# Kernel tuning notes

Hardware: AMD Instinct MI355X
Metric: run time of the kernel (lower is better)

The kernel has to match this reference:

```python
import jax, jax.numpy as jnp
import numpy as np

D, H, WIN, TEMP = 512, 8, 2, 1.0
DH = D // H
SCALE = DH ** -0.5
SHIFT = WIN // 2


def _ln(x, g, b):
    m = jnp.mean(x, -1, keepdims=True)
    v = jnp.mean(jnp.square(x - m), -1, keepdims=True)
    return (x - m) * jax.lax.rsqrt(v + 1e-5) * g + b


def _win_attn(q, k, v):
    a = jax.nn.softmax(jnp.einsum('nhqd,nhkd->nhqk', q * SCALE, k) / TEMP, axis=-1)
    return jnp.einsum('nhqk,nhkd->nhqd', a, v)


def _self_block(x, p):
    qkv_w, qkv_b, proj_w, proj_b, n1g, n1b, n2g, n2b = p
    b, t, d = x.shape
    sc = x
    xw = _ln(x, n1g, n1b).reshape(b * t // WIN, WIN, d)  # window partition
    qkv = (xw @ qkv_w + qkv_b).reshape(-1, WIN, 3, H, DH).transpose(2, 0, 3, 1, 4)
    o = _win_attn(qkv[0], qkv[1], qkv[2])
    o = o.transpose(0, 2, 1, 3).reshape(-1, WIN, d) @ proj_w + proj_b
    return _ln(o.reshape(b, t, d) + sc, n2g, n2b)  # window reverse + residual


def _self_tf(x, p):
    x = _self_block(x, p)
    x = jnp.roll(x, -SHIFT, axis=1)   # sequence_shift
    x = _self_block(x, p)
    return jnp.roll(x, SHIFT, axis=1)  # sequence_inverse_shift


def _cross_block(x, y, p):
    q_w, q_b, kv_w, kv_b, proj_w, proj_b, n1g, n1b, n2g, n2b = p
    b, t, d = x.shape
    sc = x
    xw = _ln(x, n1g, n1b).reshape(-1, WIN, d)
    yw = _ln(y, n1g, n1b).reshape(-1, WIN, d)  # shared pre_norm, as in source
    q = (xw @ q_w + q_b).reshape(-1, WIN, H, DH).transpose(0, 2, 1, 3)
    kv = (yw @ kv_w + kv_b).reshape(-1, WIN, 2, H, DH).transpose(2, 0, 3, 1, 4)
    o = _win_attn(q, kv[0], kv[1])
    o = o.transpose(0, 2, 1, 3).reshape(-1, WIN, d) @ proj_w + proj_b
    return _ln(o.reshape(b, t, d) + sc, n2g, n2b)


def _cross_tf(x, y, p):
    x = _cross_block(x, y, p)
    x = jnp.roll(x, -SHIFT, axis=1)
    x = _cross_block(x, jnp.roll(y, -SHIFT, axis=1), p)
    return jnp.roll(x, SHIFT, axis=1)


def setup_inputs() -> dict:
    key = jax.random.key(0)
    ks = iter(jax.random.split(key, 40))
    B, T = 16, 4096
    d = {
        'x': jax.random.normal(next(ks), (B, T, D), jnp.float32),
        'y': jax.random.normal(next(ks), (B, T, D), jnp.float32),
    }

    def w(shape):
        return jax.random.normal(next(ks), shape, jnp.float32) * 0.02

    for m in ('wa', 'wv'):  # within-modal audio / video
        d[m + '_qkv_w'] = w((D, 3 * D)); d[m + '_qkv_b'] = jnp.zeros((3 * D,), jnp.float32)
        d[m + '_proj_w'] = w((D, D));    d[m + '_proj_b'] = jnp.zeros((D,), jnp.float32)
        d[m + '_n1_g'] = jnp.ones((D,), jnp.float32); d[m + '_n1_b'] = jnp.zeros((D,), jnp.float32)
        d[m + '_n2_g'] = jnp.ones((D,), jnp.float32); d[m + '_n2_b'] = jnp.zeros((D,), jnp.float32)
    # shared cross-modal transformer
    d['cm_q_w'] = w((D, D));      d['cm_q_b'] = jnp.zeros((D,), jnp.float32)
    d['cm_kv_w'] = w((D, 2 * D)); d['cm_kv_b'] = jnp.zeros((2 * D,), jnp.float32)
    d['cm_proj_w'] = w((D, D));   d['cm_proj_b'] = jnp.zeros((D,), jnp.float32)
    d['cm_n1_g'] = jnp.ones((D,), jnp.float32); d['cm_n1_b'] = jnp.zeros((D,), jnp.float32)
    d['cm_n2_g'] = jnp.ones((D,), jnp.float32); d['cm_n2_b'] = jnp.zeros((D,), jnp.float32)
    return d


def reference(x, y,
              wa_qkv_w, wa_qkv_b, wa_proj_w, wa_proj_b, wa_n1_g, wa_n1_b, wa_n2_g, wa_n2_b,
              wv_qkv_w, wv_qkv_b, wv_proj_w, wv_proj_b, wv_n1_g, wv_n1_b, wv_n2_g, wv_n2_b,
              cm_q_w, cm_q_b, cm_kv_w, cm_kv_b, cm_proj_w, cm_proj_b, cm_n1_g, cm_n1_b, cm_n2_g, cm_n2_b):
    pa = (wa_qkv_w, wa_qkv_b, wa_proj_w, wa_proj_b, wa_n1_g, wa_n1_b, wa_n2_g, wa_n2_b)
    pv = (wv_qkv_w, wv_qkv_b, wv_proj_w, wv_proj_b, wv_n1_g, wv_n1_b, wv_n2_g, wv_n2_b)
    pc = (cm_q_w, cm_q_b, cm_kv_w, cm_kv_b, cm_proj_w, cm_proj_b, cm_n1_g, cm_n1_b, cm_n2_g, cm_n2_b)
    # args.s1_attn == 'all' path
    x = _self_tf(x, pa)
    y = _self_tf(y, pv)
    xc = _cross_tf(x, y, pc)
    yc = _cross_tf(y, x, pc)
    return jnp.stack([x + xc, y + yc])  # (2, B, T, D)
```

## Files before the change

### kernel.cpp

```cpp
#include <hip/hip_runtime.h>

typedef unsigned short u16;
typedef unsigned int u32;
typedef __attribute__((ext_vector_type(8))) short short8;
typedef __attribute__((ext_vector_type(4))) short short4v;
typedef __attribute__((ext_vector_type(4))) float f32x4;

#define D_MODEL 512
#define NH 8
#define TSEQ 4096
#define NB 16
#define NROWS (NB*TSEQ)
#define QK_SCALE 0.125f
#define KDIM 512
#define NKI (KDIM/32)

__device__ __forceinline__ float b2f(u16 u){
    union { float f; unsigned int i; } v; v.i = ((unsigned int)u) << 16; return v.f;
}
__device__ __forceinline__ u16 f2b(float f){
    union { float f; unsigned int i; } v; v.f = f;
    unsigned int r = v.i + 0x7FFFu + ((v.i >> 16) & 1u);
    return (u16)(r >> 16);
}

__device__ __forceinline__ void async_copy16(u16* lds, const u16* g){
    __builtin_amdgcn_global_load_lds(
        (const __attribute__((address_space(1))) u32*)g,
        (__attribute__((address_space(3))) u32*)lds, 16, 0, 0);
}

__global__ void wconv_kernel(const float* __restrict__ W, u16* __restrict__ Wt, int K, int N){
    int idx = blockIdx.x * 256 + threadIdx.x;
    if (idx >= K * N) return;
    int n = idx / K;
    int k = idx - n * K;
    Wt[idx] = f2b(W[(size_t)k * N + n]);
}

__global__ __launch_bounds__(256) void ln_kernel(
    const float* __restrict__ X, const float* __restrict__ g,
    const float* __restrict__ b, u16* __restrict__ out)
{
    int row  = blockIdx.x * 4 + (threadIdx.x >> 6);
    int lane = threadIdx.x & 63;
    size_t base = (size_t)row * D_MODEL + lane * 8;
    float4 x0 = *(const float4*)(X + base);
    float4 x1 = *(const float4*)(X + base + 4);
    float t[8] = {x0.x,x0.y,x0.z,x0.w,x1.x,x1.y,x1.z,x1.w};
    float s = 0.f, ss = 0.f;
    #pragma unroll
    for (int j = 0; j < 8; j++){ s += t[j]; ss += t[j]*t[j]; }
    #pragma unroll
    for (int m = 1; m < 64; m <<= 1){ s += __shfl_xor(s, m); ss += __shfl_xor(ss, m); }
    float mean = s * (1.f/D_MODEL);
    float var  = ss * (1.f/D_MODEL) - mean*mean;
    float rst  = rsqrtf(var + 1e-5f);
    float4 g0 = *(const float4*)(g + lane*8);
    float4 g1 = *(const float4*)(g + lane*8 + 4);
    float4 c0 = *(const float4*)(b + lane*8);
    float4 c1 = *(const float4*)(b + lane*8 + 4);
    float gv[8] = {g0.x,g0.y,g0.z,g0.w,g1.x,g1.y,g1.z,g1.w};
    float bv[8] = {c0.x,c0.y,c0.z,c0.w,c1.x,c1.y,c1.z,c1.w};
    short8 o;
    #pragma unroll
    for (int j = 0; j < 8; j++) o[j] = (short)f2b((t[j]-mean)*rst*gv[j] + bv[j]);
    *(short8*)(out + base) = o;
}

__global__ __launch_bounds__(256) void resln_kernel(
    const u16* __restrict__ P, const float* __restrict__ Xin,
    const float* __restrict__ Add,
    const float* __restrict__ g, const float* __restrict__ b,
    float* __restrict__ out,
    u16* __restrict__ lnout, const float* __restrict__ g2, const float* __restrict__ b2)
{
    int row  = blockIdx.x * 4 + (threadIdx.x >> 6);
    int lane = threadIdx.x & 63;
    size_t base = (size_t)row * D_MODEL + lane * 8;
    short8 pv = *(const short8*)(P + base);
    float4 x0 = *(const float4*)(Xin + base);
    float4 x1 = *(const float4*)(Xin + base + 4);
    float xr[8] = {x0.x,x0.y,x0.z,x0.w,x1.x,x1.y,x1.z,x1.w};
    float t[8];
    #pragma unroll
    for (int j = 0; j < 8; j++) t[j] = b2f((u16)pv[j]) + xr[j];
    float s = 0.f, ss = 0.f;
    #pragma unroll
    for (int j = 0; j < 8; j++){ s += t[j]; ss += t[j]*t[j]; }
    #pragma unroll
    for (int m = 1; m < 64; m <<= 1){ s += __shfl_xor(s, m); ss += __shfl_xor(ss, m); }
    float mean = s * (1.f/D_MODEL);
    float var  = ss * (1.f/D_MODEL) - mean*mean;
    float rst  = rsqrtf(var + 1e-5f);
    float4 g0 = *(const float4*)(g + lane*8);
    float4 g1 = *(const float4*)(g + lane*8 + 4);
    float4 c0 = *(const float4*)(b + lane*8);
    float4 c1 = *(const float4*)(b + lane*8 + 4);
    float gv[8] = {g0.x,g0.y,g0.z,g0.w,g1.x,g1.y,g1.z,g1.w};
    float bv[8] = {c0.x,c0.y,c0.z,c0.w,c1.x,c1.y,c1.z,c1.w};
    float o[8];
    #pragma unroll
    for (int j = 0; j < 8; j++) o[j] = (t[j]-mean)*rst*gv[j] + bv[j];

    if (lnout){
        float s2 = 0.f, ss2 = 0.f;
        #pragma unroll
        for (int j = 0; j < 8; j++){ s2 += o[j]; ss2 += o[j]*o[j]; }
        #pragma unroll
        for (int m = 1; m < 64; m <<= 1){ s2 += __shfl_xor(s2, m); ss2 += __shfl_xor(ss2, m); }
        float mean2 = s2 * (1.f/D_MODEL);
        float var2  = ss2 * (1.f/D_MODEL) - mean2*mean2;
        float rst2  = rsqrtf(var2 + 1e-5f);
        float4 g20 = *(const float4*)(g2 + lane*8);
        float4 g21 = *(const float4*)(g2 + lane*8 + 4);
        float4 b20 = *(const float4*)(b2 + lane*8);
        float4 b21 = *(const float4*)(b2 + lane*8 + 4);
        float g2v[8] = {g20.x,g20.y,g20.z,g20.w,g21.x,g21.y,g21.z,g21.w};
        float b2v[8] = {b20.x,b20.y,b20.z,b20.w,b21.x,b21.y,b21.z,b21.w};
        short8 lo;
        #pragma unroll
        for (int j = 0; j < 8; j++) lo[j] = (short)f2b((o[j]-mean2)*rst2*g2v[j] + b2v[j]);
        *(short8*)(lnout + base) = lo;
    }
    if (Add){
        float4 a0 = *(const float4*)(Add + base);
        float4 a1 = *(const float4*)(Add + base + 4);
        float av[8] = {a0.x,a0.y,a0.z,a0.w,a1.x,a1.y,a1.z,a1.w};
        #pragma unroll
        for (int j = 0; j < 8; j++) o[j] += av[j];
    }
    float4 r0 = {o[0],o[1],o[2],o[3]};
    float4 r1 = {o[4],o[5],o[6],o[7]};
    *(float4*)(out + base)     = r0;
    *(float4*)(out + base + 4) = r1;
}

__global__ __launch_bounds__(256) void qkvattn_kernel(
    const u16* __restrict__ A, const u16* __restrict__ Wt,
    const float* __restrict__ bias, u16* __restrict__ O, int shift)
{
    __shared__ __align__(16) u16 lds[2][20*512];
    int tid  = threadIdx.x;
    int lane = tid & 63;
    int wid  = tid >> 6;

    int bid  = blockIdx.x;
    int swz  = (bid & 7) * 512 + (bid >> 3);
    int head = swz >> 9;
    int rt   = swz & 511;
    int bt   = rt >> 5;
    int tb   = (rt & 31) * 128;

    f32x4 acc[2][12];
    f32x4 zero = {0.f,0.f,0.f,0.f};
    #pragma unroll
    for (int m = 0; m < 2; m++)
        #pragma unroll
        for (int n = 0; n < 12; n++) acc[m][n] = zero;

    int rr = lane >> 2, kc = (lane & 3) * 8;
    const u16* p[5];
    int cidb = wid * 5;
    #pragma unroll
    for (int q = 0; q < 5; q++){
        int cid = cidb + q;
        if (cid < 8){
            int i   = cid*16 + rr;
            int tok = (tb + shift + i) & (TSEQ-1);
            p[q] = A + ((size_t)bt * TSEQ + tok) * KDIM + kc;
        } else {
            int cb   = cid - 8;
            int wrow = (cb >> 2) * 512 + head*64 + (cb & 3)*16 + rr;
            p[q] = Wt + (size_t)wrow * KDIM + kc;
        }
    }

    int lrow = lane & 15;
    int lk   = (lane >> 4) * 8;
    int aoff = (wid*32 + lrow) * 32 + lk;
    int boff = 8*512 + lrow*32 + lk;

    #pragma unroll
    for (int q = 0; q < 5; q++){ async_copy16(&lds[0][(cidb+q)*512], p[q]); p[q] += 32; }
    asm volatile("s_waitcnt vmcnt(0)" ::: "memory");
    __syncthreads();

    #pragma unroll
    for (int t = 0; t < NKI; t++){
        const u16* cbuf = lds[t & 1];
        u16* nbuf = (u16*)lds[(t & 1) ^ 1];
        if (t < NKI-1){
            #pragma unroll
            for (int q = 0; q < 5; q++){ async_copy16(&nbuf[(cidb+q)*512], p[q]); p[q] += 32; }
        }
        short8 af[2], bf[12];
        #pragma unroll
        for (int m = 0; m < 2; m++) af[m] = *(const short8*)(cbuf + aoff + m*512);
        #pragma unroll
        for (int n = 0; n < 12; n++) bf[n] = *(const short8*)(cbuf + boff + n*512);
        #pragma unroll
        for (int m = 0; m < 2; m++)
            #pragma unroll
            for (int n = 0; n < 12; n++)
                acc[m][n] = __builtin_amdgcn_mfma_f32_16x16x32_bf16(af[m], bf[n], acc[m][n], 0, 0, 0);
        if (t < NKI-1){
            asm volatile("s_waitcnt vmcnt(0)" ::: "memory");
            __syncthreads();
        }
    }

    int g_ = lane >> 4, lc = lane & 15;
    float bq[4], bk[4], bv[4];
    #pragma unroll
    for (int n = 0; n < 4; n++){
        int d = head*64 + n*16 + lc;
        bq[n] = bias[d]; bk[n] = bias[512 + d]; bv[n] = bias[1024 + d];
    }
    #pragma unroll
    for (int m = 0; m < 2; m++){
        #pragma unroll
        for (int wnd = 0; wnd < 2; wnd++){
            int ja = 2*wnd, jb = ja + 1;
            float s00=0.f, s01=0.f, s10=0.f, s11=0.f;
            #pragma unroll
            for (int n = 0; n < 4; n++){
                float qa = acc[m][n][ja] + bq[n],  qb = acc[m][n][jb] + bq[n];
                float ka = acc[m][4+n][ja] + bk[n], kb = acc[m][4+n][jb] + bk[n];
                s00 += qa*ka; s01 += qa*kb; s10 += qb*ka; s11 += qb*kb;
            }
            #pragma unroll
            for (int msk = 1; msk < 16; msk <<= 1){
                s00 += __shfl_xor(s00, msk); s01 += __shfl_xor(s01, msk);
                s10 += __shfl_xor(s10, msk); s11 += __shfl_xor(s11, msk);
            }
            s00 *= QK_SCALE; s01 *= QK_SCALE; s10 *= QK_SCALE; s11 *= QK_SCALE;
            float m0 = fmaxf(s00, s01), m1 = fmaxf(s10, s11);
            float e00 = expf(s00-m0), e01 = expf(s01-m0);
            float e10 = expf(s10-m1), e11 = expf(s11-m1);
            float ia = 1.f/(e00+e01), ib = 1.f/(e10+e11);
            float a00 = e00*ia, a01 = e01*ia, a10 = e10*ib, a11 = e11*ib;
            int ra = wid*32 + m*16 + 4*g_ + ja;
            int ta = (tb + shift + ra) & (TSEQ-1);
            size_t growa = (size_t)bt * TSEQ + ta;
            size_t growb = (size_t)bt * TSEQ + ((ta + 1) & (TSEQ-1));
            #pragma unroll
            for (int n = 0; n < 4; n++){
                float va = acc[m][8+n][ja] + bv[n], vb = acc[m][8+n][jb] + bv[n];
                int col = head*64 + n*16 + lc;
                O[growa * D_MODEL + col] = f2b(a00*va + a01*vb);
                O[growb * D_MODEL + col] = f2b(a10*va + a11*vb);
            }
        }
    }
}

#define AOFc(buf,h) (((buf)*2+(h))*8192)
#define BOFc(buf,h) (32768 + ((buf)*2+(h))*8192)

__global__ __launch_bounds__(512, 2) void gemm256_kernel(
    const u16* __restrict__ A, const u16* __restrict__ Wt,
    const float* __restrict__ bias, u16* __restrict__ C, int N, int nN)
{
    __shared__ __align__(16) u16 sh[65536];
    u16* sh_ = (u16*)sh;
    const int tid = threadIdx.x, lane = tid & 63, wid = tid >> 6;
    const int wm = wid >> 2, wn = wid & 3;
    const int cpx = (int)gridDim.x >> 3;
    const int swz = ((int)blockIdx.x & 7) * cpx + ((int)blockIdx.x >> 3);
    const int row0 = (swz / nN) * 256;
    const int col0 = (swz % nN) * 256;

    f32x4 acc[8][4];
    f32x4 zero = {0.f,0.f,0.f,0.f};
    #pragma unroll
    for (int m = 0; m < 8; m++)
        #pragma unroll
        for (int n = 0; n < 4; n++) acc[m][n] = zero;

    const int lrow = lane & 15, khi = lane >> 4;
    const int swx   = (lrow & 4) << 2;
    const int kcol0 = (khi*8) ^ swx;
    const int kcol1 = (32 + khi*8) ^ swx;
    const int aR0 = AOFc(0, wm) , aR1 = AOFc(1, wm);
    const int bh  = wn >> 1;
    const int bR0 = BOFc(0, bh), bR1 = BOFc(1, bh);
    const int abase = lrow*64;
    const int bbase = (wn & 1)*4096 + lrow*64;

    const u16* Ag = A  + (size_t)row0 * KDIM;
    const u16* Bg = Wt + (size_t)col0 * KDIM;
    const int csrc = ((lane & 7) * 8) ^ (((lane >> 3) & 4) << 2);
    const int srow = wid*16 + (lane >> 3);

    short8 af[4][2], bf[4][2];

    #define STG(dstOff, gp) { \
        const u16* s1_ = (gp) + (size_t)srow*KDIM + csrc; \
        u16* d1_ = sh_ + (dstOff) + wid*1024; \
        async_copy16(d1_, s1_); \
        async_copy16(d1_ + 512, s1_ + (size_t)8*KDIM); }
    #define RDA(bufR, h) { \
        const u16* p_ = sh_ + (bufR) + abase; \
        _Pragma("unroll") \
        for (int i_ = 0; i_ < 4; i_++){ \
            af[i_][0] = *(const short8*)(p_ + ((h)*4+i_)*1024 + kcol0); \
            af[i_][1] = *(const short8*)(p_ + ((h)*4+i_)*1024 + kcol1); } }
    #define RDB(bufR, nh) { \
        const u16* p_ = sh_ + (bufR) + bbase; \
        _Pragma("unroll") \
        for (int j_ = 0; j_ < 2; j_++){ \
            bf[(nh)*2+j_][0] = *(const short8*)(p_ + ((nh)*2+j_)*1024 + kcol0); \
            bf[(nh)*2+j_][1] = *(const short8*)(p_ + ((nh)*2+j_)*1024 + kcol1); } }
    #define MM(mh, nh) { \
        __builtin_amdgcn_s_setprio(1); \
        _Pragma("unroll") \
        for (int m_ = 0; m_ < 4; m_++) \
            _Pragma("unroll") \
            for (int n_ = 0; n_ < 2; n_++){ \
                acc[(mh)*4+m_][(nh)*2+n_] = __builtin_amdgcn_mfma_f32_16x16x32_bf16(af[m_][0], bf[(nh)*2+n_][0], acc[(mh)*4+m_][(nh)*2+n_], 0,0,0); \
                acc[(mh)*4+m_][(nh)*2+n_] = __builtin_amdgcn_mfma_f32_16x16x32_bf16(af[m_][1], bf[(nh)*2+n_][1], acc[(mh)*4+m_][(nh)*2+n_], 0,0,0); } \
        __builtin_amdgcn_s_setprio(0); }
    #define BAR() { asm volatile("" ::: "memory"); __builtin_amdgcn_s_barrier(); asm volatile("" ::: "memory"); }
    #define VMW4() asm volatile("s_waitcnt vmcnt(4)" ::: "memory")
    #define VMW0() asm volatile("s_waitcnt vmcnt(0)" ::: "memory")

    STG(BOFc(0,0), Bg);
    STG(BOFc(0,1), Bg + (size_t)128*KDIM);
    STG(AOFc(0,0), Ag);
    STG(AOFc(0,1), Ag + (size_t)128*KDIM);
    STG(BOFc(1,0), Bg + 64);
    STG(BOFc(1,1), Bg + (size_t)128*KDIM + 64);
    VMW4();
    BAR();

    #pragma unroll
    for (int i = 0; i < 4; i++){
        RDA(aR0, 0); RDB(bR0, 0);
        STG(AOFc(1,0), Ag + (2*i+1)*64);
        BAR(); MM(0,0); BAR();

        RDB(bR0, 1);
        STG(AOFc(1,1), Ag + (size_t)128*KDIM + (2*i+1)*64);
        BAR(); MM(0,1); BAR();

        RDA(aR0, 1);
        if (i < 3) STG(BOFc(0,0), Bg + (2*i+2)*64);
        BAR(); MM(1,0); BAR();

        if (i < 3){ STG(BOFc(0,1), Bg + (size_t)128*KDIM + (2*i+2)*64); VMW4(); }
        else      { VMW0(); }
        BAR(); MM(1,1); BAR();

        RDA(aR1, 0); RDB(bR1, 0);
        if (i < 3) STG(AOFc(0,0), Ag + (2*i+2)*64);
        BAR(); MM(0,0); BAR();

        RDB(bR1, 1);
        if (i < 3) STG(AOFc(0,1), Ag + (size_t)128*KDIM + (2*i+2)*64);
        BAR(); MM(0,1); BAR();

        RDA(aR1, 1);
        if (i < 3) STG(BOFc(1,0), Bg + (2*i+3)*64);
        BAR(); MM(1,0); BAR();

        if (i < 3){ STG(BOFc(1,1), Bg + (size_t)128*KDIM + (2*i+3)*64); VMW4(); }
        BAR(); MM(1,1); BAR();
    }

    int g_ = lane >> 4, lc = lane & 15;
    #pragma unroll
    for (int n = 0; n < 4; n++){
        int c = col0 + wn*64 + n*16 + lc;
        float bvv = bias[c];
        #pragma unroll
        for (int m = 0; m < 8; m++){
            int r = row0 + wm*128 + m*16 + 4*g_;
            f32x4 v = acc[m][n];
            C[(size_t)(r+0) * N + c] = f2b(v[0] + bvv);
            C[(size_t)(r+1) * N + c] = f2b(v[1] + bvv);
            C[(size_t)(r+2) * N + c] = f2b(v[2] + bvv);
            C[(size_t)(r+3) * N + c] = f2b(v[3] + bvv);
        }
    }
    #undef STG
    #undef RDA
    #undef RDB
    #undef MM
    #undef BAR
    #undef VMW4
    #undef VMW0
}

__global__ __launch_bounds__(256) void attn_cross_kernel(
    const u16* __restrict__ Q, const u16* __restrict__ KV,
    u16* __restrict__ O, int shift)
{
    int tsk  = blockIdx.x * 4 + (threadIdx.x >> 6);
    int lane = threadIdx.x & 63;
    int w  = tsk >> 1;
    int hb = tsk & 1;
    int bt = w >> 11;
    int wt = w & 2047;
    int t0 = (2*wt + shift) & (TSEQ - 1);
    int t1 = (t0 + 1) & (TSEQ - 1);
    size_t g0 = (size_t)bt * TSEQ + t0;
    size_t g1 = (size_t)bt * TSEQ + t1;
    int col = hb*256 + lane*4;
    short4v q0 = *(const short4v*)(Q  + g0*512  + col);
    short4v q1 = *(const short4v*)(Q  + g1*512  + col);
    short4v k0 = *(const short4v*)(KV + g0*1024 + col);
    short4v k1 = *(const short4v*)(KV + g1*1024 + col);
    short4v v0 = *(const short4v*)(KV + g0*1024 + 512 + col);
    short4v v1 = *(const short4v*)(KV + g1*1024 + 512 + col);
    float s00=0.f, s01=0.f, s10=0.f, s11=0.f;
    float v0f[4], v1f[4];
    #pragma unroll
    for (int j = 0; j < 4; j++){
        float qa = b2f((u16)q0[j]), qb = b2f((u16)q1[j]);
        float ka = b2f((u16)k0[j]), kb = b2f((u16)k1[j]);
        v0f[j] = b2f((u16)v0[j]); v1f[j] = b2f((u16)v1[j]);
        s00 += qa*ka; s01 += qa*kb; s10 += qb*ka; s11 += qb*kb;
    }
    #pragma unroll
    for (int m = 1; m < 16; m <<= 1){
        s00 += __shfl_xor(s00, m); s01 += __shfl_xor(s01, m);
        s10 += __shfl_xor(s10, m); s11 += __shfl_xor(s11, m);
    }
    s00 *= QK_SCALE; s01 *= QK_SCALE; s10 *= QK_SCALE; s11 *= QK_SCALE;
    float m0 = fmaxf(s00, s01), m1 = fmaxf(s10, s11);
    float e00 = expf(s00 - m0), e01 = expf(s01 - m0);
    float e10 = expf(s10 - m1), e11 = expf(s11 - m1);
    float ia = 1.f/(e00 + e01), ib = 1.f/(e10 + e11);
    float a00 = e00*ia, a01 = e01*ia, a10 = e10*ib, a11 = e11*ib;
    short4v o0, o1;
    #pragma unroll
    for (int j = 0; j < 4; j++){
        o0[j] = (short)f2b(a00*v0f[j] + a01*v1f[j]);
        o1[j] = (short)f2b(a10*v0f[j] + a11*v1f[j]);
    }
    *(short4v*)(O + g0*512 + col) = o0;
    *(short4v*)(O + g1*512 + col) = o1;
}

extern "C" void kernel_launch(void* const* d_in, const int* in_sizes, int n_in,
                              void* d_out, int out_size, void* d_ws, size_t ws_size,
                              hipStream_t stream)
{
    const float* x = (const float*)d_in[0];
    const float* y = (const float*)d_in[1];
    const float* wa_qkv_w = (const float*)d_in[2];  const float* wa_qkv_b = (const float*)d_in[3];
    const float* wa_proj_w= (const float*)d_in[4];  const float* wa_proj_b= (const float*)d_in[5];
    const float* wa_n1g   = (const float*)d_in[6];  const float* wa_n1b   = (const float*)d_in[7];
    const float* wa_n2g   = (const float*)d_in[8];  const float* wa_n2b   = (const float*)d_in[9];
    const float* wv_qkv_w = (const float*)d_in[10]; const float* wv_qkv_b = (const float*)d_in[11];
    const float* wv_proj_w= (const float*)d_in[12]; const float* wv_proj_b= (const float*)d_in[13];
    const float* wv_n1g   = (const float*)d_in[14]; const float* wv_n1b   = (const float*)d_in[15];
    const float* wv_n2g   = (const float*)d_in[16]; const float* wv_n2b   = (const float*)d_in[17];
    const float* cm_q_w   = (const float*)d_in[18]; const float* cm_q_b   = (const float*)d_in[19];
    const float* cm_kv_w  = (const float*)d_in[20]; const float* cm_kv_b  = (const float*)d_in[21];
    const float* cm_proj_w= (const float*)d_in[22]; const float* cm_proj_b= (const float*)d_in[23];
    const float* cm_n1g   = (const float*)d_in[24]; const float* cm_n1b   = (const float*)d_in[25];
    const float* cm_n2g   = (const float*)d_in[26]; const float* cm_n2b   = (const float*)d_in[27];

    char* ws = (char*)d_ws;
    const size_t SZ_F32 = (size_t)NROWS * D_MODEL * 4;
    const size_t SZ_B16 = (size_t)NROWS * D_MODEL * 2;
    float* F1  = (float*)(ws);
    float* XF  = (float*)(ws + SZ_F32);
    float* YF  = (float*)(ws + 2*SZ_F32);
    u16*   XN  = (u16*)  (ws + 3*SZ_F32);
    u16*   CN  = (u16*)  (ws + 3*SZ_F32 + SZ_B16);
    u16*   XLN = (u16*)  (ws + 3*SZ_F32 + 2*SZ_B16);
    u16*   YLN = (u16*)  (ws + 3*SZ_F32 + 3*SZ_B16);
    u16*   O   = (u16*)  (ws + 3*SZ_F32 + 4*SZ_B16);
    u16*   KVb = (u16*)  (ws + 3*SZ_F32 + 5*SZ_B16);
    u16*   WB  = (u16*)  (ws + 3*SZ_F32 + 8*SZ_B16);

    u16* PB = KVb;

    u16* wa_qkv_t  = WB;
    u16* wa_proj_t = wa_qkv_t  + 1536*512;
    u16* wv_qkv_t  = wa_proj_t + 512*512;
    u16* wv_proj_t = wv_qkv_t  + 1536*512;
    u16* cm_q_t    = wv_proj_t + 512*512;
    u16* cm_kv_t   = cm_q_t    + 512*512;
    u16* cm_proj_t = cm_kv_t   + 1024*512;

    auto conv = [&](const float* W, u16* Wt, int K, int N){
        int total = K * N;
        wconv_kernel<<<(total + 255) / 256, 256, 0, stream>>>(W, Wt, K, N);
    };
    conv(wa_qkv_w,  wa_qkv_t,  512, 1536);
    conv(wa_proj_w, wa_proj_t, 512, 512);
    conv(wv_qkv_w,  wv_qkv_t,  512, 1536);
    conv(wv_proj_w, wv_proj_t, 512, 512);
    conv(cm_q_w,    cm_q_t,    512, 512);
    conv(cm_kv_w,   cm_kv_t,   512, 1024);
    conv(cm_proj_w, cm_proj_t, 512, 512);

    const int lnGrid   = NROWS / 4;
    const int attnGrid = NROWS / 2 * 2 / 4;
    const int qaGrid   = (NROWS / 128) * NH;

    auto gemm = [&](const u16* Ain, const u16* Wt, const float* bias, u16* Cout, int N){
        int nN = N / 256;
        gemm256_kernel<<<(NROWS/256) * nN, 512, 0, stream>>>(Ain, Wt, bias, Cout, N, nN);
    };

    auto self_chain = [&](const float* in, float* outF, u16* outLN,
                          const u16* qkvT, const float* qkv_b,
                          const u16* projT, const float* proj_b,
                          const float* n1g, const float* n1b,
                          const float* n2g, const float* n2b){
        ln_kernel<<<lnGrid, 256, 0, stream>>>(in, n1g, n1b, XN);
        qkvattn_kernel<<<qaGrid, 256, 0, stream>>>(XN, qkvT, qkv_b, O, 0);
        gemm(O, projT, proj_b, PB, 512);
        resln_kernel<<<lnGrid, 256, 0, stream>>>(PB, in, nullptr, n2g, n2b, F1, XN, n1g, n1b);
        qkvattn_kernel<<<qaGrid, 256, 0, stream>>>(XN, qkvT, qkv_b, O, 1);
        gemm(O, projT, proj_b, PB, 512);
        resln_kernel<<<lnGrid, 256, 0, stream>>>(PB, F1, nullptr, n2g, n2b, outF, outLN, cm_n1g, cm_n1b);
    };

    self_chain(x, XF, XLN, wa_qkv_t, wa_qkv_b, wa_proj_t, wa_proj_b, wa_n1g, wa_n1b, wa_n2g, wa_n2b);
    self_chain(y, YF, YLN, wv_qkv_t, wv_qkv_b, wv_proj_t, wv_proj_b, wv_n1g, wv_n1b, wv_n2g, wv_n2b);

    float* out0 = (float*)d_out;
    float* out1 = out0 + (size_t)NROWS * D_MODEL;

    auto cross_chain = [&](const u16* qLN, const u16* kvLN, const float* resF, float* outF){
        gemm(kvLN, cm_kv_t, cm_kv_b, KVb, 1024);
        gemm(qLN,  cm_q_t,  cm_q_b,  XN,  512);
        attn_cross_kernel<<<attnGrid, 256, 0, stream>>>(XN, KVb, O, 0);
        gemm(O, cm_proj_t, cm_proj_b, XN, 512);
        resln_kernel<<<lnGrid, 256, 0, stream>>>(XN, resF, nullptr, cm_n2g, cm_n2b, F1, CN, cm_n1g, cm_n1b);
        gemm(CN, cm_q_t, cm_q_b, XN, 512);
        attn_cross_kernel<<<attnGrid, 256, 0, stream>>>(XN, KVb, O, 1);
        gemm(O, cm_proj_t, cm_proj_b, XN, 512);
        resln_kernel<<<lnGrid, 256, 0, stream>>>(XN, F1, resF, cm_n2g, cm_n2b, outF, nullptr, nullptr, nullptr);
    };

    cross_chain(XLN, YLN, XF, out0);
    cross_chain(YLN, XLN, YF, out1);
}
```

Before: 2.357 ms.

## Fuse cross-attention Q projection with windowed attention; remap block swizzle

```diff
diff --git a/kernel.cpp b/kernel.cpp
--- a/kernel.cpp
+++ b/kernel.cpp
@@ -3,7 +3,6 @@
 typedef unsigned short u16;
 typedef unsigned int u32;
 typedef __attribute__((ext_vector_type(8))) short short8;
-typedef __attribute__((ext_vector_type(4))) short short4v;
 typedef __attribute__((ext_vector_type(4))) float f32x4;
 
 #define D_MODEL 512
@@ -145,12 +144,13 @@
     int lane = tid & 63;
     int wid  = tid >> 6;
 
-    int bid  = blockIdx.x;
-    int swz  = (bid & 7) * 512 + (bid >> 3);
-    int head = swz >> 9;
-    int rt   = swz & 511;
-    int bt   = rt >> 5;
-    int tb   = (rt & 31) * 128;
+    int bid   = blockIdx.x;
+    int xcd   = bid & 7;
+    int local = bid >> 3;
+    int head  = local & 7;
+    int rt    = xcd * 64 + (local >> 3);
+    int bt    = rt >> 5;
+    int tb    = (rt & 31) * 128;
 
     f32x4 acc[2][12];
     f32x4 zero = {0.f,0.f,0.f,0.f};
@@ -250,6 +250,129 @@
                 int col = head*64 + n*16 + lc;
                 O[growa * D_MODEL + col] = f2b(a00*va + a01*vb);
                 O[growb * D_MODEL + col] = f2b(a10*va + a11*vb);
+            }
+        }
+    }
+}
+
+__global__ __launch_bounds__(256) void qattn_kernel(
+    const u16* __restrict__ A, const u16* __restrict__ Wq,
+    const float* __restrict__ bias, const u16* __restrict__ KV,
+    u16* __restrict__ O, int shift)
+{
+    __shared__ __align__(16) u16 lds[2][12*512];
+    int tid  = threadIdx.x;
+    int lane = tid & 63;
+    int wid  = tid >> 6;
+
+    int bid   = blockIdx.x;
+    int xcd   = bid & 7;
+    int local = bid >> 3;
+    int head  = local & 7;
+    int rt    = xcd * 64 + (local >> 3);
+    int bt    = rt >> 5;
+    int tb    = (rt & 31) * 128;
+
+    f32x4 acc[2][4];
+    f32x4 zero = {0.f,0.f,0.f,0.f};
+    #pragma unroll
+    for (int m = 0; m < 2; m++)
+        #pragma unroll
+        for (int n = 0; n < 4; n++) acc[m][n] = zero;
+
+    int rr = lane >> 2, kc = (lane & 3) * 8;
+    const u16* p[3];
+    int cidb = wid * 3;
+    #pragma unroll
+    for (int q = 0; q < 3; q++){
+        int cid = cidb + q;
+        if (cid < 8){
+            int i   = cid*16 + rr;
+            int tok = (tb + shift + i) & (TSEQ-1);
+            p[q] = A + ((size_t)bt * TSEQ + tok) * KDIM + kc;
+        } else {
+            int cb = cid - 8;
+            p[q] = Wq + (size_t)(head*64 + cb*16 + rr) * KDIM + kc;
+        }
+    }
+
+    int lrow = lane & 15;
+    int lk   = (lane >> 4) * 8;
+    int aoff = (wid*32 + lrow) * 32 + lk;
+    int boff = 8*512 + lrow*32 + lk;
+
+    #pragma unroll
+    for (int q = 0; q < 3; q++){ async_copy16(&lds[0][(cidb+q)*512], p[q]); p[q] += 32; }
+    asm volatile("s_waitcnt vmcnt(0)" ::: "memory");
+    __syncthreads();
+
+    #pragma unroll
+    for (int t = 0; t < NKI; t++){
+        const u16* cbuf = lds[t & 1];
+        u16* nbuf = (u16*)lds[(t & 1) ^ 1];
+        if (t < NKI-1){
+            #pragma unroll
+            for (int q = 0; q < 3; q++){ async_copy16(&nbuf[(cidb+q)*512], p[q]); p[q] += 32; }
+        }
+        short8 af[2], bf[4];
+        #pragma unroll
+        for (int m = 0; m < 2; m++) af[m] = *(const short8*)(cbuf + aoff + m*512);
+        #pragma unroll
+        for (int n = 0; n < 4; n++) bf[n] = *(const short8*)(cbuf + boff + n*512);
+        #pragma unroll
+        for (int m = 0; m < 2; m++)
+            #pragma unroll
+            for (int n = 0; n < 4; n++)
+                acc[m][n] = __builtin_amdgcn_mfma_f32_16x16x32_bf16(af[m], bf[n], acc[m][n], 0, 0, 0);
+        if (t < NKI-1){
+            asm volatile("s_waitcnt vmcnt(0)" ::: "memory");
+            __syncthreads();
+        }
+    }
+
+    int g_ = lane >> 4, lc = lane & 15;
+    float bq[4];
+    #pragma unroll
+    for (int n = 0; n < 4; n++) bq[n] = bias[head*64 + n*16 + lc];
+
+    #pragma unroll
+    for (int m = 0; m < 2; m++){
+        #pragma unroll
+        for (int wnd = 0; wnd < 2; wnd++){
+            int ja = 2*wnd, jb = ja + 1;
+            int ra = wid*32 + m*16 + 4*g_ + ja;
+            int ta = (tb + shift + ra) & (TSEQ-1);
+            size_t g0 = (size_t)bt * TSEQ + ta;
+            size_t g1 = (size_t)bt * TSEQ + ((ta + 1) & (TSEQ-1));
+            float s00=0.f, s01=0.f, s10=0.f, s11=0.f;
+            float v0f[4], v1f[4];
+            #pragma unroll
+            for (int n = 0; n < 4; n++){
+                int col = head*64 + n*16 + lc;
+                float ka = b2f(KV[g0*1024 + col]);
+                float kb = b2f(KV[g1*1024 + col]);
+                v0f[n]   = b2f(KV[g0*1024 + 512 + col]);
+                v1f[n]   = b2f(KV[g1*1024 + 512 + col]);
+                float qa = acc[m][n][ja] + bq[n];
+                float qb = acc[m][n][jb] + bq[n];
+                s00 += qa*ka; s01 += qa*kb; s10 += qb*ka; s11 += qb*kb;
+            }
+            #pragma unroll
+            for (int msk = 1; msk < 16; msk <<= 1){
+                s00 += __shfl_xor(s00, msk); s01 += __shfl_xor(s01, msk);
+                s10 += __shfl_xor(s10, msk); s11 += __shfl_xor(s11, msk);
+            }
+            s00 *= QK_SCALE; s01 *= QK_SCALE; s10 *= QK_SCALE; s11 *= QK_SCALE;
+            float m0 = fmaxf(s00, s01), m1 = fmaxf(s10, s11);
+            float e00 = expf(s00-m0), e01 = expf(s01-m0);
+            float e10 = expf(s10-m1), e11 = expf(s11-m1);
+            float ia = 1.f/(e00+e01), ib = 1.f/(e10+e11);
+            float a00 = e00*ia, a01 = e01*ia, a10 = e10*ib, a11 = e11*ib;
+            #pragma unroll
+            for (int n = 0; n < 4; n++){
+                int col = head*64 + n*16 + lc;
+                O[g0 * D_MODEL + col] = f2b(a00*v0f[n] + a01*v1f[n]);
+                O[g1 * D_MODEL + col] = f2b(a10*v0f[n] + a11*v1f[n]);
             }
         }
     }
@@ -392,57 +515,6 @@
     #undef VMW0
 }
 
-__global__ __launch_bounds__(256) void attn_cross_kernel(
-    const u16* __restrict__ Q, const u16* __restrict__ KV,
-    u16* __restrict__ O, int shift)
-{
-    int tsk  = blockIdx.x * 4 + (threadIdx.x >> 6);
-    int lane = threadIdx.x & 63;
-    int w  = tsk >> 1;
-    int hb = tsk & 1;
-    int bt = w >> 11;
-    int wt = w & 2047;
-    int t0 = (2*wt + shift) & (TSEQ - 1);
-    int t1 = (t0 + 1) & (TSEQ - 1);
-    size_t g0 = (size_t)bt * TSEQ + t0;
-    size_t g1 = (size_t)bt * TSEQ + t1;
-    int col = hb*256 + lane*4;
-    short4v q0 = *(const short4v*)(Q  + g0*512  + col);
-    short4v q1 = *(const short4v*)(Q  + g1*512  + col);
-    short4v k0 = *(const short4v*)(KV + g0*1024 + col);
-    short4v k1 = *(const short4v*)(KV + g1*1024 + col);
-    short4v v0 = *(const short4v*)(KV + g0*1024 + 512 + col);
-    short4v v1 = *(const short4v*)(KV + g1*1024 + 512 + col);
-    float s00=0.f, s01=0.f, s10=0.f, s11=0.f;
-    float v0f[4], v1f[4];
-    #pragma unroll
-    for (int j = 0; j < 4; j++){
-        float qa = b2f((u16)q0[j]), qb = b2f((u16)q1[j]);
-        float ka = b2f((u16)k0[j]), kb = b2f((u16)k1[j]);
-        v0f[j] = b2f((u16)v0[j]); v1f[j] = b2f((u16)v1[j]);
-        s00 += qa*ka; s01 += qa*kb; s10 += qb*ka; s11 += qb*kb;
-    }
-    #pragma unroll
-    for (int m = 1; m < 16; m <<= 1){
-        s00 += __shfl_xor(s00, m); s01 += __shfl_xor(s01, m);
-        s10 += __shfl_xor(s10, m); s11 += __shfl_xor(s11, m);
-    }
-    s00 *= QK_SCALE; s01 *= QK_SCALE; s10 *= QK_SCALE; s11 *= QK_SCALE;
-    float m0 = fmaxf(s00, s01), m1 = fmaxf(s10, s11);
-    float e00 = expf(s00 - m0), e01 = expf(s01 - m0);
-    float e10 = expf(s10 - m1), e11 = expf(s11 - m1);
-    float ia = 1.f/(e00 + e01), ib = 1.f/(e10 + e11);
-    float a00 = e00*ia, a01 = e01*ia, a10 = e10*ib, a11 = e11*ib;
-    short4v o0, o1;
-    #pragma unroll
-    for (int j = 0; j < 4; j++){
-        o0[j] = (short)f2b(a00*v0f[j] + a01*v1f[j]);
-        o1[j] = (short)f2b(a10*v0f[j] + a11*v1f[j]);
-    }
-    *(short4v*)(O + g0*512 + col) = o0;
-    *(short4v*)(O + g1*512 + col) = o1;
-}
-
 extern "C" void kernel_launch(void* const* d_in, const int* in_sizes, int n_in,
                               void* d_out, int out_size, void* d_ws, size_t ws_size,
                               hipStream_t stream)
@@ -499,9 +571,8 @@
     conv(cm_kv_w,   cm_kv_t,   512, 1024);
     conv(cm_proj_w, cm_proj_t, 512, 512);
 
-    const int lnGrid   = NROWS / 4;
-    const int attnGrid = NROWS / 2 * 2 / 4;
-    const int qaGrid   = (NROWS / 128) * NH;
+    const int lnGrid = NROWS / 4;
+    const int qaGrid = (NROWS / 128) * NH;
 
     auto gemm = [&](const u16* Ain, const u16* Wt, const float* bias, u16* Cout, int N){
         int nN = N / 256;
@@ -530,12 +601,10 @@
 
     auto cross_chain = [&](const u16* qLN, const u16* kvLN, const float* resF, float* outF){
         gemm(kvLN, cm_kv_t, cm_kv_b, KVb, 1024);
-        gemm(qLN,  cm_q_t,  cm_q_b,  XN,  512);
-        attn_cross_kernel<<<attnGrid, 256, 0, stream>>>(XN, KVb, O, 0);
+        qattn_kernel<<<qaGrid, 256, 0, stream>>>(qLN, cm_q_t, cm_q_b, KVb, O, 0);
         gemm(O, cm_proj_t, cm_proj_b, XN, 512);
         resln_kernel<<<lnGrid, 256, 0, stream>>>(XN, resF, nullptr, cm_n2g, cm_n2b, F1, CN, cm_n1g, cm_n1b);
-        gemm(CN, cm_q_t, cm_q_b, XN, 512);
-        attn_cross_kernel<<<attnGrid, 256, 0, stream>>>(XN, KVb, O, 1);
+        qattn_kernel<<<qaGrid, 256, 0, stream>>>(CN, cm_q_t, cm_q_b, KVb, O, 1);
         gemm(O, cm_proj_t, cm_proj_b, XN, 512);
         resln_kernel<<<lnGrid, 256, 0, stream>>>(XN, F1, resF, cm_n2g, cm_n2b, outF, nullptr, nullptr, nullptr);
     };
```

Result: slower. 2.502 ms (+6.2%).
